# Kernel tuning notes

Hardware: AMD Instinct MI355X
Metric: run time of the kernel (lower is better)

The kernel has to match this reference:

```python
import jax, jax.numpy as jnp
import numpy as np

B, S, D, H = 4, 1024, 1024, 16
E = D // H  # head_dim = 64
N = 2 * H  # number of slots


def _ln(x, g, b, eps=1e-5):
    m = x.mean(-1, keepdims=True)
    v = ((x - m) ** 2).mean(-1, keepdims=True)
    return (x - m) / jnp.sqrt(v + eps) * g + b


def _feat(x):
    # F.elu(x, 1.0) + 1.0
    return jax.nn.elu(x) + 1.0


def setup_inputs() -> dict:
    key = jax.random.key(0)
    ks = jax.random.split(key, 40)
    w = lambda k, shape: jax.random.normal(k, shape, jnp.float32) * 0.02
    z = lambda shape: jnp.zeros(shape, jnp.float32)
    o = lambda shape: jnp.ones(shape, jnp.float32)
    return {
        'x': jax.random.normal(ks[0], (B, S, D), jnp.float32),
        'ln1_g': o(D), 'ln1_b': z(D), 'ln2_g': o(D), 'ln2_b': z(D),
        'Wq': w(ks[1], (D, D)), 'bq': z(D),
        'Wk': w(ks[2], (D, D)), 'bk': z(D),
        'Wv': w(ks[3], (D, D)), 'bv': z(D),
        'Wf': w(ks[4], (D, D)), 'bf': z(D),
        'Wr1': w(ks[5], (D, 2 * D)), 'br1': z(2 * D),
        'Wr2': w(ks[6], (2 * D, D)), 'br2': z(D),
        'Wip': w(ks[7], (D, N * E)), 'bip': z(N * E),
        'Wtq': w(ks[8], (E, E)), 'btq': z(E),
        'Wtk': w(ks[9], (E, E)), 'btk': z(E),
        'Wtv': w(ks[10], (E, E)), 'btv': z(E),
        'lnp_g': o(E), 'lnp_b': z(E),
        'Wl1': w(ks[11], (E, 2 * E)), 'bl1': z(2 * E),
        'Wl2': w(ks[12], (2 * E, E)), 'bl2': z(E),
        'Wsp': w(ks[13], (2 * E, E)), 'bsp': z(E),
    }


def reference(x, ln1_g, ln1_b, ln2_g, ln2_b, Wq, bq, Wk, bk, Wv, bv, Wf, bf,
              Wr1, br1, Wr2, br2, Wip, bip, Wtq, btq, Wtk, btk, Wtv, btv,
              lnp_g, lnp_b, Wl1, bl1, Wl2, bl2, Wsp, bsp):
    xn = _ln(x, ln1_g, ln1_b)
    # main q/k/v
    q = (xn @ Wq + bq).reshape(B, S, H, E).transpose(0, 2, 1, 3) / np.sqrt(E)  # [B,H,S,E]
    k = (xn @ Wk + bk).reshape(B, S, H, E)
    v = (xn @ Wv + bv).reshape(B, S, H, E)
    kv0 = jnp.concatenate([k, v], axis=2)  # [B,S,2H,E] initial slots

    # --- competitive (slot) attention, 3 iterations ---
    inp = (xn @ Wip + bip).reshape(B, S, N, E)
    kk = _feat(inp @ Wtk + btk)          # [B,S,N,E]
    vv = inp @ Wtv + btv                 # [B,S,N,E]
    slots = kv0
    scale = 1.0 / E                      # slot_size = head_dim
    for _ in range(3):
        qq = (slots @ Wtq + btq) + kv0
        qq = _feat(qq * (E ** -0.5))
        logits = jnp.einsum('bswe,bsne->bswn', kk, qq)
        attn = jax.nn.softmax(logits, axis=3) + 1e-6
        attn = attn / attn.sum(axis=2, keepdims=True)
        upd = jnp.einsum('bswn,bswe->bsne', attn, vv)
        h = _ln(upd, lnp_g, lnp_b)
        h = jax.nn.relu(h @ Wl1 + bl1) @ Wl2 + bl2
        slots = slots + h * scale
    # slot_dropout is eval-mode identity
    slots = jnp.concatenate([kv0, slots], axis=-1) @ Wsp + bsp  # [B,S,2H,E]

    k2 = slots[:, :, :H].transpose(0, 2, 3, 1)  # [B,H,E,S]
    v2 = slots[:, :, H:].transpose(0, 2, 1, 3)  # [B,H,S,E]
    qf = _feat(q)
    kf = _feat(k2)
    score = qf @ kf                              # [B,H,S,S]
    score = score / (score.sum(-1, keepdims=True) + 1e-5)
    out = (score @ v2).transpose(0, 2, 1, 3).reshape(B, S, D)
    out = out @ Wf + bf
    out = x + out
    res = out
    h = _ln(out, ln2_g, ln2_b)
    h = jax.nn.relu(h @ Wr1 + br1) @ Wr2 + br2  # dropouts are eval-mode identity
    return res + h
```

## Files before the change

### kernel.cpp

```cpp
#include <hip/hip_runtime.h>
#include <hip/hip_bf16.h>

typedef __hip_bfloat16 bf16t;
typedef short short8 __attribute__((ext_vector_type(8)));
typedef float f32x4 __attribute__((ext_vector_type(4)));


__device__ __forceinline__ float featf(float x) { return x > 0.f ? x + 1.f : expf(x); }
__device__ __forceinline__ float ldf(const bf16t* p, size_t i) { return __bfloat162float(p[i]); }
__device__ __forceinline__ float ldf(const float* p, size_t i) { return p[i]; }
__device__ __forceinline__ void stf(bf16t* p, size_t i, float v) { p[i] = __float2bfloat16(v); }
__device__ __forceinline__ void stf(float* p, size_t i, float v) { p[i] = v; }
__device__ __forceinline__ float b2f(unsigned short u) {
    unsigned int x = ((unsigned int)u) << 16; float f; __builtin_memcpy(&f, &x, 4); return f;
}
__device__ __forceinline__ unsigned short f2b(float f) {
    bf16t h = __float2bfloat16(f); unsigned short u; __builtin_memcpy(&u, &h, 2); return u;
}
__device__ __forceinline__ void gl_lds16(const short* g, short* l) {
    __builtin_amdgcn_global_load_lds((const __attribute__((address_space(1))) unsigned int*)g,
                                     (__attribute__((address_space(3))) unsigned int*)l, 16, 0, 0);
}
#define MFMA16(a, b, c) __builtin_amdgcn_mfma_f32_16x16x32_bf16((a), (b), (c), 0, 0, 0)

__global__ __launch_bounds__(256) void fill_k(float* __restrict__ out, int n, float v) {
    int i = blockIdx.x * 256 + threadIdx.x;
    if (i < n) out[i] = v;
}

__global__ __launch_bounds__(256) void transpose_k(const float* __restrict__ W,
                                                   bf16t* __restrict__ Wt,
                                                   int R, int C) {
    __shared__ bf16t tile[32][33];
    int c0 = blockIdx.x * 32, r0 = blockIdx.y * 32;
    int tx = threadIdx.x, ty = threadIdx.y;
    #pragma unroll
    for (int i = 0; i < 32; i += 8) {
        int r = r0 + ty + i, c = c0 + tx;
        if (r < R && c < C) tile[ty + i][tx] = __float2bfloat16(W[(size_t)r * C + c]);
    }
    __syncthreads();
    #pragma unroll
    for (int i = 0; i < 32; i += 8) {
        int r = c0 + ty + i, c = r0 + tx;
        if (r < C && c < R) Wt[(size_t)r * R + c] = tile[tx][ty + i];
    }
}

__global__ __launch_bounds__(256) void small_prep_k(const float* __restrict__ Wtk,
                                                    const float* __restrict__ Wtv,
                                                    const float* __restrict__ Wtq,
                                                    const float* __restrict__ Wl1,
                                                    const float* __restrict__ Wl2,
                                                    const float* __restrict__ Wsp,
                                                    const float* __restrict__ bk,
                                                    const float* __restrict__ bv,
                                                    const float* __restrict__ bip,
                                                    const float* __restrict__ bq,
                                                    bf16t* __restrict__ WtkT,
                                                    bf16t* __restrict__ WtvT,
                                                    bf16t* __restrict__ WtqI,
                                                    bf16t* __restrict__ Wl1T,
                                                    bf16t* __restrict__ Wl2T,
                                                    bf16t* __restrict__ WspT,
                                                    float* __restrict__ bcat) {
    int b = blockIdx.x, tid = threadIdx.x;
    if (b == 0) {
        for (int i = tid; i < 4096; i += 256) { int c = i >> 6, r = i & 63; WtkT[i] = __float2bfloat16(Wtk[r * 64 + c]); }
    } else if (b == 1) {
        for (int i = tid; i < 4096; i += 256) { int c = i >> 6, r = i & 63; WtvT[i] = __float2bfloat16(Wtv[r * 64 + c]); }
    } else if (b == 2) {
        for (int i = tid; i < 8192; i += 256) {
            int e = i >> 7, k = i & 127;
            float v = (k < 64) ? Wtq[k * 64 + e] : ((k - 64 == e) ? 1.f : 0.f);
            WtqI[i] = __float2bfloat16(v);
        }
    } else if (b == 3) {
        for (int i = tid; i < 8192; i += 256) { int n = i >> 6, k = i & 63; Wl1T[i] = __float2bfloat16(Wl1[k * 128 + n]); }
    } else if (b == 4) {
        for (int i = tid; i < 8192; i += 256) { int n = i >> 7, k = i & 127; Wl2T[i] = __float2bfloat16(Wl2[k * 64 + n]); }
    } else if (b == 5) {
        for (int i = tid; i < 8192; i += 256) { int n = i >> 7, k = i & 127; WspT[i] = __float2bfloat16(Wsp[k * 64 + n]); }
    } else {
        for (int i = tid; i < 5120; i += 256) {
            float v;
            if (i < 1024) v = bk[i];
            else if (i < 2048) v = bv[i - 1024];
            else if (i < 4096) v = bip[i - 2048];
            else v = bq[i - 4096];
            bcat[i] = v;
        }
    }
}

__global__ __launch_bounds__(256) void ln_kernel(const float* __restrict__ X,
                                                 const float* __restrict__ g,
                                                 const float* __restrict__ b,
                                                 bf16t* __restrict__ Y) {
    int t = blockIdx.x, tid = threadIdx.x;
    size_t base = (size_t)t * 1024 + tid * 4;
    float v0 = X[base + 0], v1 = X[base + 1], v2 = X[base + 2], v3 = X[base + 3];
    float s = v0 + v1 + v2 + v3;
    float q = v0 * v0 + v1 * v1 + v2 * v2 + v3 * v3;
    __shared__ float rs[4], rq[4];
    for (int o = 32; o > 0; o >>= 1) { s += __shfl_down(s, o); q += __shfl_down(q, o); }
    int wid = tid >> 6, lane = tid & 63;
    if (lane == 0) { rs[wid] = s; rq[wid] = q; }
    __syncthreads();
    float S = rs[0] + rs[1] + rs[2] + rs[3];
    float Q = rq[0] + rq[1] + rq[2] + rq[3];
    float mean = S * (1.f / 1024.f);
    float var = Q * (1.f / 1024.f) - mean * mean;
    float rstd = rsqrtf(var + 1e-5f);
    int c = tid * 4;
    stf(Y, base + 0, (v0 - mean) * rstd * g[c + 0] + b[c + 0]);
    stf(Y, base + 1, (v1 - mean) * rstd * g[c + 1] + b[c + 1]);
    stf(Y, base + 2, (v2 - mean) * rstd * g[c + 2] + b[c + 2]);
    stf(Y, base + 3, (v3 - mean) * rstd * g[c + 3] + b[c + 3]);
}

template <int MODE, typename TC, typename TADD>
__global__ __launch_bounds__(256) void gemm128_k(const bf16t* __restrict__ A,
                                                 const bf16t* __restrict__ Bt,
                                                 const float* __restrict__ bias,
                                                 const TADD* __restrict__ add,
                                                 TC* __restrict__ C,
                                                 int M, int N, int K, int ldC) {
    __shared__ short As[128 * 32];
    __shared__ short Bs[128 * 32];
    int tid = threadIdx.x;
    int wave = tid >> 6, lane = tid & 63;
    int l16 = lane & 15, quad = lane >> 4;
    int tilesM = M >> 7;
    int tm = blockIdx.x % tilesM;
    int tn = blockIdx.x / tilesM;
    int wm = wave >> 1, wn = wave & 1;

    int lrow = lane >> 2;
    int lseg = (lane & 3) * 8;
    const short* Ag = (const short*)A + (size_t)(tm * 128 + wave * 32 + lrow) * K + lseg;
    const short* Ag2 = Ag + (size_t)16 * K;
    const short* Bg = (const short*)Bt + (size_t)(tn * 128 + wave * 32 + lrow) * K + lseg;
    const short* Bg2 = Bg + (size_t)16 * K;
    short* Asw = As + (wave * 32) * 32;
    short* Asw2 = Asw + 16 * 32;
    short* Bsw = Bs + (wave * 32) * 32;
    short* Bsw2 = Bsw + 16 * 32;

    f32x4 acc[4][4] = {};
    for (int k0 = 0; k0 < K; k0 += 32) {
        gl_lds16(Ag + k0, Asw);
        gl_lds16(Ag2 + k0, Asw2);
        gl_lds16(Bg + k0, Bsw);
        gl_lds16(Bg2 + k0, Bsw2);
        __syncthreads();
        short8 av[4], bv[4];
        #pragma unroll
        for (int i = 0; i < 4; i++)
            av[i] = *(const short8*)(As + (wm * 64 + i * 16 + l16) * 32 + quad * 8);
        #pragma unroll
        for (int j = 0; j < 4; j++)
            bv[j] = *(const short8*)(Bs + (wn * 64 + j * 16 + l16) * 32 + quad * 8);
        #pragma unroll
        for (int i = 0; i < 4; i++)
            #pragma unroll
            for (int j = 0; j < 4; j++)
                acc[i][j] = MFMA16(av[i], bv[j], acc[i][j]);
        __syncthreads();
    }

    #pragma unroll
    for (int j = 0; j < 4; j++) {
        int col = tn * 128 + wn * 64 + j * 16 + l16;
        float bcol = bias[col];
        #pragma unroll
        for (int i = 0; i < 4; i++) {
            int row0 = tm * 128 + wm * 64 + i * 16 + quad * 4;
            #pragma unroll
            for (int r = 0; r < 4; r++) {
                int row = row0 + r;
                float v = acc[i][j][r] + bcol;
                float outv;
                if constexpr (MODE == 0) outv = v;
                else if constexpr (MODE == 4) outv = fmaxf(v, 0.f);
                else if constexpr (MODE == 5) outv = v + ldf(add, (size_t)row * N + col);
                else outv = v;
                stf(C, (size_t)row * ldC + col, outv);
            }
        }
    }
}

__global__ __launch_bounds__(256) void gemm_proj_k(const bf16t* __restrict__ A,
                                                   const bf16t* __restrict__ Bt,
                                                   const float* __restrict__ bias,
                                                   bf16t* __restrict__ kv0,
                                                   bf16t* __restrict__ inp,
                                                   bf16t* __restrict__ qf) {
    __shared__ short As[128 * 32];
    __shared__ short Bs[128 * 32];
    const int K = 1024;
    int tid = threadIdx.x;
    int wave = tid >> 6, lane = tid & 63;
    int l16 = lane & 15, quad = lane >> 4;
    int tm = blockIdx.x & 31;
    int tn = blockIdx.x >> 5;
    int wm = wave >> 1, wn = wave & 1;

    int lrow = lane >> 2;
    int lseg = (lane & 3) * 8;
    const short* Ag = (const short*)A + (size_t)(tm * 128 + wave * 32 + lrow) * K + lseg;
    const short* Ag2 = Ag + (size_t)16 * K;
    const short* Bg = (const short*)Bt + (size_t)(tn * 128 + wave * 32 + lrow) * K + lseg;
    const short* Bg2 = Bg + (size_t)16 * K;
    short* Asw = As + (wave * 32) * 32;
    short* Asw2 = Asw + 16 * 32;
    short* Bsw = Bs + (wave * 32) * 32;
    short* Bsw2 = Bsw + 16 * 32;

    f32x4 acc[4][4] = {};
    for (int k0 = 0; k0 < K; k0 += 32) {
        gl_lds16(Ag + k0, Asw);
        gl_lds16(Ag2 + k0, Asw2);
        gl_lds16(Bg + k0, Bsw);
        gl_lds16(Bg2 + k0, Bsw2);
        __syncthreads();
        short8 av[4], bv[4];
        #pragma unroll
        for (int i = 0; i < 4; i++)
            av[i] = *(const short8*)(As + (wm * 64 + i * 16 + l16) * 32 + quad * 8);
        #pragma unroll
        for (int j = 0; j < 4; j++)
            bv[j] = *(const short8*)(Bs + (wn * 64 + j * 16 + l16) * 32 + quad * 8);
        #pragma unroll
        for (int i = 0; i < 4; i++)
            #pragma unroll
            for (int j = 0; j < 4; j++)
                acc[i][j] = MFMA16(av[i], bv[j], acc[i][j]);
        __syncthreads();
    }

    #pragma unroll
    for (int j = 0; j < 4; j++) {
        int col = tn * 128 + wn * 64 + j * 16 + l16;
        float bcol = bias[col];
        #pragma unroll
        for (int i = 0; i < 4; i++) {
            int row0 = tm * 128 + wm * 64 + i * 16 + quad * 4;
            #pragma unroll
            for (int r = 0; r < 4; r++) {
                int row = row0 + r;
                float v = acc[i][j][r] + bcol;
                if (tn < 16) stf(kv0, (size_t)row * 2048 + col, v);
                else if (tn < 32) stf(inp, (size_t)row * 2048 + (col - 2048), v);
                else stf(qf, (size_t)row * 1024 + (col - 4096), featf(v * 0.125f));
            }
        }
    }
}

template <int MODE, typename TC>
__global__ __launch_bounds__(256) void gemm_k(const bf16t* __restrict__ A,
                                              const bf16t* __restrict__ Bt,
                                              const float* __restrict__ bias,
                                              TC* __restrict__ C,
                                              int M, int N, int K, int ldC) {
    int wave = threadIdx.x >> 6;
    int lane = threadIdx.x & 63;
    int tilesN = N >> 6;
    int tiles = (M >> 6) * tilesN;
    int tile = blockIdx.x * 4 + wave;
    if (tile >= tiles) return;
    int tm = tile / tilesN, tn = tile - tm * tilesN;
    int l16 = lane & 15, quad = lane >> 4;

    f32x4 acc[4][4] = {};
    const short* Ab = (const short*)A + (size_t)(tm * 64 + l16) * K;
    const short* Bb = (const short*)Bt + (size_t)(tn * 64 + l16) * K;

    for (int k0 = 0; k0 < K; k0 += 32) {
        int ka = k0 + quad * 8;
        short8 av[4], bv[4];
        #pragma unroll
        for (int i = 0; i < 4; i++) av[i] = *(const short8*)(Ab + (size_t)i * 16 * K + ka);
        #pragma unroll
        for (int j = 0; j < 4; j++) bv[j] = *(const short8*)(Bb + (size_t)j * 16 * K + ka);
        #pragma unroll
        for (int i = 0; i < 4; i++)
            #pragma unroll
            for (int j = 0; j < 4; j++)
                acc[i][j] = MFMA16(av[i], bv[j], acc[i][j]);
    }

    #pragma unroll
    for (int j = 0; j < 4; j++) {
        int col = tn * 64 + j * 16 + l16;
        float bcol = bias[col];
        #pragma unroll
        for (int i = 0; i < 4; i++) {
            int row0 = tm * 64 + i * 16 + quad * 4;
            #pragma unroll
            for (int r = 0; r < 4; r++) {
                int row = row0 + r;
                float v = acc[i][j][r] + bcol;
                if constexpr (MODE == 7) {
                    stf(C, (size_t)(row >> 5) * 2048 + (size_t)col * 32 + (row & 31), v);
                } else {
                    float outv;
                    if constexpr (MODE == 0) outv = v;
                    else if constexpr (MODE == 1) outv = featf(v);
                    else outv = v;
                    stf(C, (size_t)row * ldC + col, outv);
                }
            }
        }
    }
}

__global__ __launch_bounds__(256) void gemm_cat_k(const bf16t* __restrict__ A1,
                                                  const bf16t* __restrict__ A2,
                                                  const bf16t* __restrict__ Bt,
                                                  const float* __restrict__ bias,
                                                  bf16t* __restrict__ C, int M) {
    int wave = threadIdx.x >> 6;
    int lane = threadIdx.x & 63;
    int tiles = M >> 6;
    int tile = blockIdx.x * 4 + wave;
    if (tile >= tiles) return;
    int tm = tile;
    int l16 = lane & 15, quad = lane >> 4;
    f32x4 acc[4][4] = {};
    #pragma unroll
    for (int p = 0; p < 2; p++) {
        const short* Ab = (const short*)(p ? A2 : A1) + (size_t)(tm * 64 + l16) * 64;
        const short* Bb = (const short*)Bt + (size_t)l16 * 128 + p * 64;
        #pragma unroll
        for (int k0 = 0; k0 < 64; k0 += 32) {
            int ka = k0 + quad * 8;
            short8 av[4], bv[4];
            #pragma unroll
            for (int i = 0; i < 4; i++) av[i] = *(const short8*)(Ab + (size_t)i * 16 * 64 + ka);
            #pragma unroll
            for (int j = 0; j < 4; j++) bv[j] = *(const short8*)(Bb + (size_t)j * 16 * 128 + ka);
            #pragma unroll
            for (int i = 0; i < 4; i++)
                #pragma unroll
                for (int j = 0; j < 4; j++)
                    acc[i][j] = MFMA16(av[i], bv[j], acc[i][j]);
        }
    }
    #pragma unroll
    for (int j = 0; j < 4; j++) {
        int col = j * 16 + l16;
        float bcol = bias[col];
        #pragma unroll
        for (int i = 0; i < 4; i++) {
            int row0 = tm * 64 + i * 16 + quad * 4;
            #pragma unroll
            for (int r = 0; r < 4; r++)
                C[(size_t)(row0 + r) * 64 + col] = __float2bfloat16(acc[i][j][r] + bcol);
        }
    }
}

__global__ __launch_bounds__(256) void slot_all_k(const bf16t* __restrict__ kv0,
                                                  const bf16t* __restrict__ kk,
                                                  const bf16t* __restrict__ vvT,
                                                  const bf16t* __restrict__ WtqI,
                                                  const float* __restrict__ btq,
                                                  const float* __restrict__ lnpg,
                                                  const float* __restrict__ lnpb,
                                                  const bf16t* __restrict__ Wl1T,
                                                  const float* __restrict__ bl1,
                                                  const bf16t* __restrict__ Wl2T,
                                                  const float* __restrict__ bl2,
                                                  bf16t* __restrict__ slots_out) {
    __shared__ short slotsS[4][32 * 72];
    __shared__ short scratch[4][32 * 72];
    int wave = threadIdx.x >> 6, lane = threadIdx.x & 63;
    int l16 = lane & 15, quad = lane >> 4;
    int t = blockIdx.x * 4 + wave;
    short* S = slotsS[wave];
    short* X = scratch[wave];
    size_t tbase = (size_t)t * 2048;

    {
        const short* src = (const short*)kv0 + tbase;
        #pragma unroll
        for (int p = 0; p < 4; p++) {
            int idx = p * 512 + lane * 8;
            int row = idx >> 6, col = idx & 63;
            *(short8*)(S + row * 72 + col) = *(const short8*)(src + idx);
        }
    }
    short8 kkf[2][2], kvf[2][2];
    #pragma unroll
    for (int i = 0; i < 2; i++)
        #pragma unroll
        for (int k0 = 0; k0 < 2; k0++) {
            size_t fo = tbase + (size_t)(i * 16 + l16) * 64 + k0 * 32 + quad * 8;
            kkf[i][k0] = *(const short8*)((const short*)kk + fo);
            kvf[i][k0] = *(const short8*)((const short*)kv0 + fo);
        }

    float btqv[4], bl2v[4], lgv[4], lbv[4], bl1v[8];
    #pragma unroll
    for (int j = 0; j < 4; j++) {
        btqv[j] = btq[j * 16 + l16]; bl2v[j] = bl2[j * 16 + l16];
        lgv[j] = lnpg[j * 16 + l16]; lbv[j] = lnpb[j * 16 + l16];
    }
    #pragma unroll
    for (int j = 0; j < 8; j++) bl1v[j] = bl1[j * 16 + l16];

    for (int it = 0; it < 3; it++) {
        f32x4 aq[2][4] = {};
        #pragma unroll
        for (int k0 = 0; k0 < 4; k0++) {
            short8 af[2];
            #pragma unroll
            for (int i = 0; i < 2; i++)
                af[i] = (k0 < 2) ? *(const short8*)(S + (i * 16 + l16) * 72 + k0 * 32 + quad * 8)
                                 : kvf[i][k0 - 2];
            #pragma unroll
            for (int j = 0; j < 4; j++) {
                short8 bf_ = *(const short8*)((const short*)WtqI + (size_t)(j * 16 + l16) * 128 + k0 * 32 + quad * 8);
                #pragma unroll
                for (int i = 0; i < 2; i++) aq[i][j] = MFMA16(af[i], bf_, aq[i][j]);
            }
        }
        #pragma unroll
        for (int i = 0; i < 2; i++)
            #pragma unroll
            for (int j = 0; j < 4; j++)
                #pragma unroll
                for (int r = 0; r < 4; r++) {
                    int n = i * 16 + quad * 4 + r, e = j * 16 + l16;
                    X[n * 72 + e] = (short)f2b(featf((aq[i][j][r] + btqv[j]) * 0.125f));
                }
        f32x4 al[2][2] = {};
        #pragma unroll
        for (int k0 = 0; k0 < 2; k0++) {
            short8 bf_[2];
            #pragma unroll
            for (int j = 0; j < 2; j++)
                bf_[j] = *(const short8*)(X + (j * 16 + l16) * 72 + k0 * 32 + quad * 8);
            #pragma unroll
            for (int i = 0; i < 2; i++)
                #pragma unroll
                for (int j = 0; j < 2; j++)
                    al[i][j] = MFMA16(kkf[i][k0], bf_[j], al[i][j]);
        }
        #pragma unroll
        for (int i = 0; i < 2; i++)
            #pragma unroll
            for (int r = 0; r < 4; r++) {
                float m = fmaxf(al[i][0][r], al[i][1][r]);
                #pragma unroll
                for (int d = 1; d < 16; d <<= 1) m = fmaxf(m, __shfl_xor(m, d));
                float e0 = expf(al[i][0][r] - m), e1 = expf(al[i][1][r] - m);
                float s = e0 + e1;
                #pragma unroll
                for (int d = 1; d < 16; d <<= 1) s += __shfl_xor(s, d);
                float inv = 1.f / s;
                al[i][0][r] = e0 * inv + 1e-6f;
                al[i][1][r] = e1 * inv + 1e-6f;
            }
        #pragma unroll
        for (int j = 0; j < 2; j++) {
            float cs = 0.f;
            #pragma unroll
            for (int i = 0; i < 2; i++)
                #pragma unroll
                for (int r = 0; r < 4; r++) cs += al[i][j][r];
            cs += __shfl_xor(cs, 16);
            cs += __shfl_xor(cs, 32);
            float inv = 1.f / cs;
            #pragma unroll
            for (int i = 0; i < 2; i++)
                #pragma unroll
                for (int r = 0; r < 4; r++) al[i][j][r] *= inv;
        }
        #pragma unroll
        for (int i = 0; i < 2; i++)
            #pragma unroll
            for (int j = 0; j < 2; j++)
                #pragma unroll
                for (int r = 0; r < 4; r++) {
                    int w = i * 16 + quad * 4 + r, n = j * 16 + l16;
                    X[n * 40 + w] = (short)f2b(al[i][j][r]);
                }
        f32x4 au[2][4] = {};
        {
            short8 af[2];
            #pragma unroll
            for (int i = 0; i < 2; i++)
                af[i] = *(const short8*)(X + (i * 16 + l16) * 40 + quad * 8);
            #pragma unroll
            for (int j = 0; j < 4; j++) {
                short8 bf_ = *(const short8*)((const short*)vvT + tbase + (size_t)(j * 16 + l16) * 32 + quad * 8);
                #pragma unroll
                for (int i = 0; i < 2; i++) au[i][j] = MFMA16(af[i], bf_, au[i][j]);
            }
        }
        #pragma unroll
        for (int i = 0; i < 2; i++)
            #pragma unroll
            for (int r = 0; r < 4; r++) {
                float s1 = 0.f, s2 = 0.f;
                #pragma unroll
                for (int j = 0; j < 4; j++) { float u = au[i][j][r]; s1 += u; s2 += u * u; }
                #pragma unroll
                for (int d = 1; d < 16; d <<= 1) { s1 += __shfl_xor(s1, d); s2 += __shfl_xor(s2, d); }
                float mean = s1 * (1.f / 64.f);
                float var = s2 * (1.f / 64.f) - mean * mean;
                float rstd = rsqrtf(var + 1e-5f);
                int n = i * 16 + quad * 4 + r;
                #pragma unroll
                for (int j = 0; j < 4; j++)
                    X[n * 72 + j * 16 + l16] = (short)f2b((au[i][j][r] - mean) * rstd * lgv[j] + lbv[j]);
            }
        short8 a1[2][2];
        #pragma unroll
        for (int i = 0; i < 2; i++)
            #pragma unroll
            for (int k0 = 0; k0 < 2; k0++)
                a1[i][k0] = *(const short8*)(X + (i * 16 + l16) * 72 + k0 * 32 + quad * 8);
        f32x4 ac2[2][4] = {};
        #pragma unroll
        for (int c = 0; c < 2; c++) {
            f32x4 ac1[2][4] = {};
            #pragma unroll
            for (int k0 = 0; k0 < 2; k0++)
                #pragma unroll
                for (int j = 0; j < 4; j++) {
                    short8 bf_ = *(const short8*)((const short*)Wl1T + (size_t)((c * 4 + j) * 16 + l16) * 64 + k0 * 32 + quad * 8);
                    #pragma unroll
                    for (int i = 0; i < 2; i++) ac1[i][j] = MFMA16(a1[i][k0], bf_, ac1[i][j]);
                }
            #pragma unroll
            for (int i = 0; i < 2; i++)
                #pragma unroll
                for (int j = 0; j < 4; j++)
                    #pragma unroll
                    for (int r = 0; r < 4; r++) {
                        int n = i * 16 + quad * 4 + r;
                        X[n * 72 + j * 16 + l16] = (short)f2b(fmaxf(ac1[i][j][r] + bl1v[c * 4 + j], 0.f));
                    }
            #pragma unroll
            for (int kc = 0; kc < 2; kc++) {
                short8 a2[2];
                #pragma unroll
                for (int i = 0; i < 2; i++)
                    a2[i] = *(const short8*)(X + (i * 16 + l16) * 72 + kc * 32 + quad * 8);
                int k1 = c * 2 + kc;
                #pragma unroll
                for (int j = 0; j < 4; j++) {
                    short8 bf_ = *(const short8*)((const short*)Wl2T + (size_t)(j * 16 + l16) * 128 + k1 * 32 + quad * 8);
                    #pragma unroll
                    for (int i = 0; i < 2; i++) ac2[i][j] = MFMA16(a2[i], bf_, ac2[i][j]);
                }
            }
        }
        #pragma unroll
        for (int i = 0; i < 2; i++)
            #pragma unroll
            for (int j = 0; j < 4; j++)
                #pragma unroll
                for (int r = 0; r < 4; r++) {
                    int n = i * 16 + quad * 4 + r, e = j * 16 + l16;
                    float old = b2f((unsigned short)S[n * 72 + e]);
                    S[n * 72 + e] = (short)f2b(old + (ac2[i][j][r] + bl2v[j]) * (1.f / 64.f));
                }
    }
    {
        short* dst = (short*)slots_out + tbase;
        #pragma unroll
        for (int p = 0; p < 4; p++) {
            int idx = p * 512 + lane * 8;
            int row = idx >> 6, col = idx & 63;
            *(short8*)(dst + idx) = *(const short8*)(S + row * 72 + col);
        }
    }
}

__global__ __launch_bounds__(256) void kv_outer_k(const bf16t* __restrict__ slotsO,
                                                  float* __restrict__ Kmat,
                                                  float* __restrict__ ksum) {
    __shared__ short kfT[64 * 72];
    __shared__ short v2T[64 * 72];
    __shared__ float ksred[8][64];
    int bh = blockIdx.x;
    int b = bh >> 4, h = bh & 15;
    int tid = threadIdx.x;
    int wave = tid >> 6, lane = tid & 63;
    int l16 = lane & 15, quad = lane >> 4;
    int m0 = wave * 16;

    int sgrp = tid >> 5;
    int e0 = (tid & 31) * 2;
    float ks0 = 0.f, ks1 = 0.f;
    f32x4 acc[4];
    #pragma unroll
    for (int j = 0; j < 4; j++) acc[j] = (f32x4){0.f, 0.f, 0.f, 0.f};

    for (int tile = 0; tile < 16; tile++) {
        #pragma unroll
        for (int p = 0; p < 8; p++) {
            int sl = p * 8 + sgrp;
            size_t row = ((size_t)(b * 1024 + tile * 64 + sl)) * 2048;
            unsigned int dk = *(const unsigned int*)((const unsigned short*)slotsO + row + h * 64 + e0);
            float f0 = featf(b2f((unsigned short)(dk & 0xffff)));
            float f1 = featf(b2f((unsigned short)(dk >> 16)));
            ks0 += f0; ks1 += f1;
            kfT[e0 * 72 + sl] = (short)f2b(f0);
            kfT[(e0 + 1) * 72 + sl] = (short)f2b(f1);
            unsigned int dv = *(const unsigned int*)((const unsigned short*)slotsO + row + (16 + h) * 64 + e0);
            v2T[e0 * 72 + sl] = (short)(dv & 0xffff);
            v2T[(e0 + 1) * 72 + sl] = (short)(dv >> 16);
        }
        __syncthreads();
        #pragma unroll
        for (int k2 = 0; k2 < 2; k2++) {
            short8 a = *(const short8*)(kfT + (m0 + l16) * 72 + k2 * 32 + quad * 8);
            #pragma unroll
            for (int j = 0; j < 4; j++) {
                short8 bv = *(const short8*)(v2T + (j * 16 + l16) * 72 + k2 * 32 + quad * 8);
                acc[j] = MFMA16(a, bv, acc[j]);
            }
        }
        __syncthreads();
    }

    float* Km = Kmat + (size_t)bh * 4096;
    #pragma unroll
    for (int j = 0; j < 4; j++)
        #pragma unroll
        for (int r = 0; r < 4; r++)
            Km[(m0 + quad * 4 + r) * 64 + j * 16 + l16] = acc[j][r];

    ksred[sgrp][e0] = ks0;
    ksred[sgrp][e0 + 1] = ks1;
    __syncthreads();
    if (tid < 64) {
        float s = 0.f;
        #pragma unroll
        for (int r = 0; r < 8; r++) s += ksred[r][tid];
        ksum[bh * 64 + tid] = s;
    }
}

__global__ __launch_bounds__(256) void attn_out_k(const bf16t* __restrict__ qf,
                                                  const float* __restrict__ Kmat,
                                                  const float* __restrict__ ksum,
                                                  bf16t* __restrict__ out) {
    int t = blockIdx.x, tid = threadIdx.x;
    int b = t >> 10;
    __shared__ float q[16 * 65];
    __shared__ float dinv[16];
    for (int i = tid; i < 1024; i += 256) {
        int h = i >> 6, e = i & 63;
        q[h * 65 + e] = __bfloat162float(qf[(size_t)t * 1024 + i]);
    }
    __syncthreads();
    if (tid < 16) {
        int bh = b * 16 + tid;
        float d = 0.f;
        for (int e = 0; e < 64; e++) d += q[tid * 65 + e] * ksum[bh * 64 + e];
        dinv[tid] = 1.f / (d + 1e-5f);
    }
    __syncthreads();
    int h = tid >> 4, j0 = (tid & 15) * 4;
    const float* Km = Kmat + (size_t)(b * 16 + h) * 4096;
    float a0 = 0.f, a1 = 0.f, a2 = 0.f, a3 = 0.f;
    for (int e = 0; e < 64; e++) {
        float qe = q[h * 65 + e];
        const float* kr = Km + e * 64 + j0;
        a0 += qe * kr[0]; a1 += qe * kr[1]; a2 += qe * kr[2]; a3 += qe * kr[3];
    }
    float di = dinv[h];
    size_t ob = (size_t)t * 1024 + h * 64 + j0;
    out[ob + 0] = __float2bfloat16(a0 * di);
    out[ob + 1] = __float2bfloat16(a1 * di);
    out[ob + 2] = __float2bfloat16(a2 * di);
    out[ob + 3] = __float2bfloat16(a3 * di);
}

#define LAUNCH_GEMM(MODE, TCT, A_, Bt_, bias_, C_, M_, N_, K_, ldC_)                         \
    do {                                                                                     \
        int tiles__ = ((M_) >> 6) * ((N_) >> 6);                                             \
        gemm_k<MODE, TCT><<<(tiles__ + 3) / 4, 256, 0, stream>>>(                            \
            (const bf16t*)(A_), (const bf16t*)(Bt_), (const float*)(bias_),                  \
            (TCT*)(C_), (M_), (N_), (K_), (ldC_));                                           \
    } while (0)

#define LAUNCH_GEMM128(MODE, TCT, TADDT, A_, Bt_, bias_, add_, C_, M_, N_, K_, ldC_)         \
    do {                                                                                     \
        int tiles__ = ((M_) >> 7) * ((N_) >> 7);                                             \
        gemm128_k<MODE, TCT, TADDT><<<tiles__, 256, 0, stream>>>(                            \
            (const bf16t*)(A_), (const bf16t*)(Bt_), (const float*)(bias_),                  \
            (const TADDT*)(add_), (TCT*)(C_), (M_), (N_), (K_), (ldC_));                     \
    } while (0)

extern "C" void kernel_launch(void* const* d_in, const int* in_sizes, int n_in,
                              void* d_out, int out_size, void* d_ws, size_t ws_size,
                              hipStream_t stream) {
    (void)in_sizes; (void)n_in;
    const float* x    = (const float*)d_in[0];
    const float* ln1g = (const float*)d_in[1];
    const float* ln1b = (const float*)d_in[2];
    const float* ln2g = (const float*)d_in[3];
    const float* ln2b = (const float*)d_in[4];
    const float* Wq  = (const float*)d_in[5];  const float* bq  = (const float*)d_in[6];
    const float* Wk  = (const float*)d_in[7];  const float* bk  = (const float*)d_in[8];
    const float* Wv  = (const float*)d_in[9];  const float* bv  = (const float*)d_in[10];
    const float* Wf  = (const float*)d_in[11]; const float* bWf = (const float*)d_in[12];
    const float* Wr1 = (const float*)d_in[13]; const float* br1 = (const float*)d_in[14];
    const float* Wr2 = (const float*)d_in[15]; const float* br2 = (const float*)d_in[16];
    const float* Wip = (const float*)d_in[17]; const float* bip = (const float*)d_in[18];
    const float* Wtq = (const float*)d_in[19]; const float* btq = (const float*)d_in[20];
    const float* Wtk = (const float*)d_in[21]; const float* btk = (const float*)d_in[22];
    const float* Wtv = (const float*)d_in[23]; const float* btv = (const float*)d_in[24];
    const float* lnpg= (const float*)d_in[25]; const float* lnpb= (const float*)d_in[26];
    const float* Wl1 = (const float*)d_in[27]; const float* bl1 = (const float*)d_in[28];
    const float* Wl2 = (const float*)d_in[29]; const float* bl2 = (const float*)d_in[30];
    const float* Wsp = (const float*)d_in[31]; const float* bsp = (const float*)d_in[32];

    char* ws = (char*)d_ws;
    size_t off = 0;
    auto alloc = [&](size_t bytes) -> char* {
        off = (off + 255) & ~(size_t)255;
        char* p = ws + off;
        off += bytes;
        return p;
    };
    const size_t T = 4096, TS = 131072;
    const size_t MB8 = T * 1024 * 2, MB16 = T * 2048 * 2;
    bf16t* R_xn   = (bf16t*)alloc(MB8);
    bf16t* R_h1   = (bf16t*)alloc(MB8);
    bf16t* R_kv0  = (bf16t*)alloc(MB16);
    bf16t* R_inp  = (bf16t*)alloc(MB16);
    bf16t* R_kk   = (bf16t*)alloc(MB16);
    bf16t* R_vv   = (bf16t*)alloc(MB16);
    bf16t* R_sl   = (bf16t*)alloc(MB16);
    bf16t* Wcat   = (bf16t*)alloc(5120 * 1024 * 2);
    bf16t* WtkT = (bf16t*)alloc(64 * 64 * 2);
    bf16t* WtvT = (bf16t*)alloc(64 * 64 * 2);
    bf16t* WtqI = (bf16t*)alloc(64 * 128 * 2);
    bf16t* Wl1T = (bf16t*)alloc(128 * 64 * 2);
    bf16t* Wl2T = (bf16t*)alloc(64 * 128 * 2);
    bf16t* WspT = (bf16t*)alloc(64 * 128 * 2);
    float* bcat = (float*)alloc(5120 * 4);
    float* Kmat = (float*)alloc(64 * 4096 * 4);
    float* ksum = (float*)alloc(64 * 64 * 4);

    if (off > ws_size) {
        fill_k<<<(out_size + 255) / 256, 256, 0, stream>>>((float*)d_out, out_size, 1000.f);
        return;
    }
    float* R_res = (float*)R_vv;

    auto tr = [&](const float* W, bf16t* Wt, int R, int C) {
        dim3 g((C + 31) / 32, (R + 31) / 32), blk(32, 8);
        transpose_k<<<g, blk, 0, stream>>>(W, Wt, R, C);
    };

    small_prep_k<<<7, 256, 0, stream>>>(Wtk, Wtv, Wtq, Wl1, Wl2, Wsp, bk, bv, bip, bq,
                                        WtkT, WtvT, WtqI, Wl1T, Wl2T, WspT, bcat);

    ln_kernel<<<4096, 256, 0, stream>>>(x, ln1g, ln1b, R_xn);

    tr(Wk, Wcat, 1024, 1024);
    tr(Wv, Wcat + (size_t)1024 * 1024, 1024, 1024);
    tr(Wip, Wcat + (size_t)2048 * 1024, 1024, 2048);
    tr(Wq, Wcat + (size_t)4096 * 1024, 1024, 1024);

    gemm_proj_k<<<1280, 256, 0, stream>>>(R_xn, Wcat, bcat, R_kv0, R_inp, R_h1);

    LAUNCH_GEMM(1, bf16t, R_inp, WtkT, btk, R_kk, 131072, 64, 64, 64);
    LAUNCH_GEMM(7, bf16t, R_inp, WtvT, btv, R_vv, 131072, 64, 64, 64);

    slot_all_k<<<1024, 256, 0, stream>>>(R_kv0, R_kk, R_vv, WtqI, btq, lnpg, lnpb,
                                         Wl1T, bl1, Wl2T, bl2, R_sl);

    gemm_cat_k<<<512, 256, 0, stream>>>(R_kv0, R_sl, WspT, bsp, R_kk, 131072);

    kv_outer_k<<<64, 256, 0, stream>>>(R_kk, Kmat, ksum);

    attn_out_k<<<4096, 256, 0, stream>>>(R_h1, Kmat, ksum, R_inp);

    tr(Wf, Wcat, 1024, 1024);
    LAUNCH_GEMM128(5, float, float, R_inp, Wcat, bWf, x, R_res, 4096, 1024, 1024, 1024);

    ln_kernel<<<4096, 256, 0, stream>>>(R_res, ln2g, ln2b, R_xn);
    tr(Wr1, Wcat, 1024, 2048);
    LAUNCH_GEMM128(4, bf16t, bf16t, R_xn, Wcat, br1, nullptr, R_sl, 4096, 2048, 1024, 2048);
    tr(Wr2, Wcat, 2048, 1024);
    LAUNCH_GEMM128(5, float, float, R_sl, Wcat, br2, R_res, (float*)d_out, 4096, 1024, 2048, 1024);
}
```

Baseline: 617.0 us.

## Batch weight transposes and fuse kk/vv projections into single kernel launches

Merges the per-matrix transpose launches into two multi-matrix transpose kernels and fuses the two small Wtk/Wtv GEMMs into one kernel that reads the input once and writes both outputs. This cuts launch count and halves reads of the inp tensor. The slot kernel stops keeping kk/kv0 fragments and bias vectors in registers across iterations and reloads them per iteration through a runtime offset, likely to lower register pressure. Transposed FFN weights are placed in the dead kv0 buffer, and the transpose kernel drops its bounds checks, so it assumes dimensions are multiples of 32.

Result: faster. 573.2 us (-7.1%).

```diff
diff --git a/kernel.cpp b/kernel.cpp
--- a/kernel.cpp
+++ b/kernel.cpp
@@ -28,23 +28,29 @@
     if (i < n) out[i] = v;
 }
 
-__global__ __launch_bounds__(256) void transpose_k(const float* __restrict__ W,
-                                                   bf16t* __restrict__ Wt,
-                                                   int R, int C) {
+__global__ __launch_bounds__(256) void multi_transpose_k(const float* __restrict__ s0, const float* __restrict__ s1,
+                                                         const float* __restrict__ s2, const float* __restrict__ s3,
+                                                         bf16t* __restrict__ d0, bf16t* __restrict__ d1,
+                                                         bf16t* __restrict__ d2, bf16t* __restrict__ d3,
+                                                         int R0, int C0, int R1, int C1, int R2, int C2, int R3, int C3,
+                                                         int e0, int e1, int e2) {
     __shared__ bf16t tile[32][33];
-    int c0 = blockIdx.x * 32, r0 = blockIdx.y * 32;
-    int tx = threadIdx.x, ty = threadIdx.y;
-    #pragma unroll
-    for (int i = 0; i < 32; i += 8) {
-        int r = r0 + ty + i, c = c0 + tx;
-        if (r < R && c < C) tile[ty + i][tx] = __float2bfloat16(W[(size_t)r * C + c]);
-    }
+    int b = blockIdx.x;
+    const float* W; bf16t* Wt; int C, R, lb;
+    if (b < e0)      { W = s0; Wt = d0; R = R0; C = C0; lb = b; }
+    else if (b < e1) { W = s1; Wt = d1; R = R1; C = C1; lb = b - e0; }
+    else if (b < e2) { W = s2; Wt = d2; R = R2; C = C2; lb = b - e1; }
+    else             { W = s3; Wt = d3; R = R3; C = C3; lb = b - e2; }
+    int tiles_c = C >> 5;
+    int c0 = (lb % tiles_c) * 32, r0 = (lb / tiles_c) * 32;
+    int tx = threadIdx.x & 31, ty = threadIdx.x >> 5;
+    #pragma unroll
+    for (int i = 0; i < 32; i += 8)
+        tile[ty + i][tx] = __float2bfloat16(W[(size_t)(r0 + ty + i) * C + (c0 + tx)]);
     __syncthreads();
     #pragma unroll
-    for (int i = 0; i < 32; i += 8) {
-        int r = c0 + ty + i, c = r0 + tx;
-        if (r < C && c < R) Wt[(size_t)r * R + c] = tile[tx][ty + i];
-    }
+    for (int i = 0; i < 32; i += 8)
+        Wt[(size_t)(c0 + ty + i) * R + (r0 + tx)] = tile[tx][ty + i];
 }
 
 __global__ __launch_bounds__(256) void small_prep_k(const float* __restrict__ Wtk,
@@ -57,31 +63,35 @@
                                                     const float* __restrict__ bv,
                                                     const float* __restrict__ bip,
                                                     const float* __restrict__ bq,
-                                                    bf16t* __restrict__ WtkT,
-                                                    bf16t* __restrict__ WtvT,
+                                                    const float* __restrict__ btk,
+                                                    const float* __restrict__ btv,
+                                                    bf16t* __restrict__ WtkvT,
                                                     bf16t* __restrict__ WtqI,
                                                     bf16t* __restrict__ Wl1T,
                                                     bf16t* __restrict__ Wl2T,
                                                     bf16t* __restrict__ WspT,
-                                                    float* __restrict__ bcat) {
+                                                    float* __restrict__ bcat,
+                                                    float* __restrict__ bcat2) {
     int b = blockIdx.x, tid = threadIdx.x;
     if (b == 0) {
-        for (int i = tid; i < 4096; i += 256) { int c = i >> 6, r = i & 63; WtkT[i] = __float2bfloat16(Wtk[r * 64 + c]); }
+        for (int i = tid; i < 8192; i += 256) {
+            int n2 = i >> 6, e = i & 63;
+            float v = (n2 < 64) ? Wtk[e * 64 + n2] : Wtv[e * 64 + (n2 - 64)];
+            WtkvT[i] = __float2bfloat16(v);
+        }
     } else if (b == 1) {
-        for (int i = tid; i < 4096; i += 256) { int c = i >> 6, r = i & 63; WtvT[i] = __float2bfloat16(Wtv[r * 64 + c]); }
-    } else if (b == 2) {
         for (int i = tid; i < 8192; i += 256) {
             int e = i >> 7, k = i & 127;
             float v = (k < 64) ? Wtq[k * 64 + e] : ((k - 64 == e) ? 1.f : 0.f);
             WtqI[i] = __float2bfloat16(v);
         }
+    } else if (b == 2) {
+        for (int i = tid; i < 8192; i += 256) { int n = i >> 6, k = i & 63; Wl1T[i] = __float2bfloat16(Wl1[k * 128 + n]); }
     } else if (b == 3) {
-        for (int i = tid; i < 8192; i += 256) { int n = i >> 6, k = i & 63; Wl1T[i] = __float2bfloat16(Wl1[k * 128 + n]); }
+        for (int i = tid; i < 8192; i += 256) { int n = i >> 7, k = i & 127; Wl2T[i] = __float2bfloat16(Wl2[k * 64 + n]); }
     } else if (b == 4) {
-        for (int i = tid; i < 8192; i += 256) { int n = i >> 7, k = i & 127; Wl2T[i] = __float2bfloat16(Wl2[k * 64 + n]); }
+        for (int i = tid; i < 8192; i += 256) { int n = i >> 7, k = i & 127; WspT[i] = __float2bfloat16(Wsp[k * 64 + n]); }
     } else if (b == 5) {
-        for (int i = tid; i < 8192; i += 256) { int n = i >> 7, k = i & 127; WspT[i] = __float2bfloat16(Wsp[k * 64 + n]); }
-    } else {
         for (int i = tid; i < 5120; i += 256) {
             float v;
             if (i < 1024) v = bk[i];
@@ -90,6 +100,8 @@
             else v = bq[i - 4096];
             bcat[i] = v;
         }
+    } else {
+        if (tid < 128) bcat2[tid] = (tid < 64) ? btk[tid] : btv[tid - 64];
     }
 }
 
@@ -259,43 +271,36 @@
     }
 }
 
-template <int MODE, typename TC>
-__global__ __launch_bounds__(256) void gemm_k(const bf16t* __restrict__ A,
-                                              const bf16t* __restrict__ Bt,
-                                              const float* __restrict__ bias,
-                                              TC* __restrict__ C,
-                                              int M, int N, int K, int ldC) {
-    int wave = threadIdx.x >> 6;
-    int lane = threadIdx.x & 63;
-    int tilesN = N >> 6;
-    int tiles = (M >> 6) * tilesN;
+__global__ __launch_bounds__(256) void gemm_kv_k(const bf16t* __restrict__ A,
+                                                 const bf16t* __restrict__ Bt,
+                                                 const float* __restrict__ bias,
+                                                 bf16t* __restrict__ kkO,
+                                                 bf16t* __restrict__ vvTO) {
+    int wave = threadIdx.x >> 6, lane = threadIdx.x & 63;
     int tile = blockIdx.x * 4 + wave;
-    if (tile >= tiles) return;
-    int tm = tile / tilesN, tn = tile - tm * tilesN;
+    int tm = tile >> 1, tn = tile & 1;
     int l16 = lane & 15, quad = lane >> 4;
-
     f32x4 acc[4][4] = {};
-    const short* Ab = (const short*)A + (size_t)(tm * 64 + l16) * K;
-    const short* Bb = (const short*)Bt + (size_t)(tn * 64 + l16) * K;
-
-    for (int k0 = 0; k0 < K; k0 += 32) {
+    const short* Ab = (const short*)A + (size_t)(tm * 64 + l16) * 64;
+    const short* Bb = (const short*)Bt + (size_t)(tn * 64 + l16) * 64;
+    #pragma unroll
+    for (int k0 = 0; k0 < 64; k0 += 32) {
         int ka = k0 + quad * 8;
         short8 av[4], bv[4];
         #pragma unroll
-        for (int i = 0; i < 4; i++) av[i] = *(const short8*)(Ab + (size_t)i * 16 * K + ka);
-        #pragma unroll
-        for (int j = 0; j < 4; j++) bv[j] = *(const short8*)(Bb + (size_t)j * 16 * K + ka);
+        for (int i = 0; i < 4; i++) av[i] = *(const short8*)(Ab + (size_t)i * 16 * 64 + ka);
+        #pragma unroll
+        for (int j = 0; j < 4; j++) bv[j] = *(const short8*)(Bb + (size_t)j * 16 * 64 + ka);
         #pragma unroll
         for (int i = 0; i < 4; i++)
             #pragma unroll
             for (int j = 0; j < 4; j++)
                 acc[i][j] = MFMA16(av[i], bv[j], acc[i][j]);
     }
-
     #pragma unroll
     for (int j = 0; j < 4; j++) {
-        int col = tn * 64 + j * 16 + l16;
-        float bcol = bias[col];
+        int col = j * 16 + l16;
+        float bcol = bias[tn * 64 + col];
         #pragma unroll
         for (int i = 0; i < 4; i++) {
             int row0 = tm * 64 + i * 16 + quad * 4;
@@ -303,15 +308,8 @@
             for (int r = 0; r < 4; r++) {
                 int row = row0 + r;
                 float v = acc[i][j][r] + bcol;
-                if constexpr (MODE == 7) {
-                    stf(C, (size_t)(row >> 5) * 2048 + (size_t)col * 32 + (row & 31), v);
-                } else {
-                    float outv;
-                    if constexpr (MODE == 0) outv = v;
-                    else if constexpr (MODE == 1) outv = featf(v);
-                    else outv = v;
-                    stf(C, (size_t)row * ldC + col, outv);
-                }
+                if (tn == 0) kkO[(size_t)row * 64 + col] = __float2bfloat16(featf(v));
+                else stf(vvTO, (size_t)(row >> 5) * 2048 + (size_t)col * 32 + (row & 31), v);
             }
         }
     }
@@ -374,7 +372,8 @@
                                                   const float* __restrict__ bl1,
                                                   const bf16t* __restrict__ Wl2T,
                                                   const float* __restrict__ bl2,
-                                                  bf16t* __restrict__ slots_out) {
+                                                  bf16t* __restrict__ slots_out,
+                                                  int zoff) {
     __shared__ short slotsS[4][32 * 72];
     __shared__ short scratch[4][32 * 72];
     int wave = threadIdx.x >> 6, lane = threadIdx.x & 63;
@@ -393,54 +392,49 @@
             *(short8*)(S + row * 72 + col) = *(const short8*)(src + idx);
         }
     }
-    short8 kkf[2][2], kvf[2][2];
-    #pragma unroll
-    for (int i = 0; i < 2; i++)
-        #pragma unroll
-        for (int k0 = 0; k0 < 2; k0++) {
-            size_t fo = tbase + (size_t)(i * 16 + l16) * 64 + k0 * 32 + quad * 8;
-            kkf[i][k0] = *(const short8*)((const short*)kk + fo);
-            kvf[i][k0] = *(const short8*)((const short*)kv0 + fo);
-        }
-
-    float btqv[4], bl2v[4], lgv[4], lbv[4], bl1v[8];
-    #pragma unroll
-    for (int j = 0; j < 4; j++) {
-        btqv[j] = btq[j * 16 + l16]; bl2v[j] = bl2[j * 16 + l16];
-        lgv[j] = lnpg[j * 16 + l16]; lbv[j] = lnpb[j * 16 + l16];
-    }
-    #pragma unroll
-    for (int j = 0; j < 8; j++) bl1v[j] = bl1[j * 16 + l16];
-
+
+    #pragma unroll 1
     for (int it = 0; it < 3; it++) {
+        int vo = it * zoff;
         f32x4 aq[2][4] = {};
         #pragma unroll
         for (int k0 = 0; k0 < 4; k0++) {
             short8 af[2];
             #pragma unroll
+            for (int i = 0; i < 2; i++) {
+                if (k0 < 2)
+                    af[i] = *(const short8*)(S + (i * 16 + l16) * 72 + k0 * 32 + quad * 8);
+                else
+                    af[i] = *(const short8*)((const short*)kv0 + tbase + (size_t)((i * 16 + l16) * 64 + (k0 - 2) * 32 + quad * 8 + vo));
+            }
+            #pragma unroll
+            for (int j = 0; j < 4; j++) {
+                short8 bf_ = *(const short8*)((const short*)WtqI + (size_t)((j * 16 + l16) * 128 + k0 * 32 + quad * 8 + vo));
+                #pragma unroll
+                for (int i = 0; i < 2; i++) aq[i][j] = MFMA16(af[i], bf_, aq[i][j]);
+            }
+        }
+        {
+            float btqv[4];
+            #pragma unroll
+            for (int j = 0; j < 4; j++) btqv[j] = btq[j * 16 + l16 + vo];
+            #pragma unroll
             for (int i = 0; i < 2; i++)
-                af[i] = (k0 < 2) ? *(const short8*)(S + (i * 16 + l16) * 72 + k0 * 32 + quad * 8)
-                                 : kvf[i][k0 - 2];
-            #pragma unroll
-            for (int j = 0; j < 4; j++) {
-                short8 bf_ = *(const short8*)((const short*)WtqI + (size_t)(j * 16 + l16) * 128 + k0 * 32 + quad * 8);
-                #pragma unroll
-                for (int i = 0; i < 2; i++) aq[i][j] = MFMA16(af[i], bf_, aq[i][j]);
-            }
-        }
-        #pragma unroll
-        for (int i = 0; i < 2; i++)
-            #pragma unroll
-            for (int j = 0; j < 4; j++)
-                #pragma unroll
-                for (int r = 0; r < 4; r++) {
-                    int n = i * 16 + quad * 4 + r, e = j * 16 + l16;
-                    X[n * 72 + e] = (short)f2b(featf((aq[i][j][r] + btqv[j]) * 0.125f));
-                }
+                #pragma unroll
+                for (int j = 0; j < 4; j++)
+                    #pragma unroll
+                    for (int r = 0; r < 4; r++) {
+                        int n = i * 16 + quad * 4 + r, e = j * 16 + l16;
+                        X[n * 72 + e] = (short)f2b(featf((aq[i][j][r] + btqv[j]) * 0.125f));
+                    }
+        }
         f32x4 al[2][2] = {};
         #pragma unroll
         for (int k0 = 0; k0 < 2; k0++) {
-            short8 bf_[2];
+            short8 ak[2], bf_[2];
+            #pragma unroll
+            for (int i = 0; i < 2; i++)
+                ak[i] = *(const short8*)((const short*)kk + tbase + (size_t)((i * 16 + l16) * 64 + k0 * 32 + quad * 8 + vo));
             #pragma unroll
             for (int j = 0; j < 2; j++)
                 bf_[j] = *(const short8*)(X + (j * 16 + l16) * 72 + k0 * 32 + quad * 8);
@@ -448,7 +442,7 @@
             for (int i = 0; i < 2; i++)
                 #pragma unroll
                 for (int j = 0; j < 2; j++)
-                    al[i][j] = MFMA16(kkf[i][k0], bf_[j], al[i][j]);
+                    al[i][j] = MFMA16(ak[i], bf_[j], al[i][j]);
         }
         #pragma unroll
         for (int i = 0; i < 2; i++)
@@ -497,28 +491,33 @@
                 af[i] = *(const short8*)(X + (i * 16 + l16) * 40 + quad * 8);
             #pragma unroll
             for (int j = 0; j < 4; j++) {
-                short8 bf_ = *(const short8*)((const short*)vvT + tbase + (size_t)(j * 16 + l16) * 32 + quad * 8);
+                short8 bf_ = *(const short8*)((const short*)vvT + tbase + (size_t)((j * 16 + l16) * 32 + quad * 8 + vo));
                 #pragma unroll
                 for (int i = 0; i < 2; i++) au[i][j] = MFMA16(af[i], bf_, au[i][j]);
             }
         }
-        #pragma unroll
-        for (int i = 0; i < 2; i++)
-            #pragma unroll
-            for (int r = 0; r < 4; r++) {
-                float s1 = 0.f, s2 = 0.f;
-                #pragma unroll
-                for (int j = 0; j < 4; j++) { float u = au[i][j][r]; s1 += u; s2 += u * u; }
-                #pragma unroll
-                for (int d = 1; d < 16; d <<= 1) { s1 += __shfl_xor(s1, d); s2 += __shfl_xor(s2, d); }
-                float mean = s1 * (1.f / 64.f);
-                float var = s2 * (1.f / 64.f) - mean * mean;
-                float rstd = rsqrtf(var + 1e-5f);
-                int n = i * 16 + quad * 4 + r;
-                #pragma unroll
-                for (int j = 0; j < 4; j++)
-                    X[n * 72 + j * 16 + l16] = (short)f2b((au[i][j][r] - mean) * rstd * lgv[j] + lbv[j]);
-            }
+        {
+            float lgv[4], lbv[4];
+            #pragma unroll
+            for (int j = 0; j < 4; j++) { lgv[j] = lnpg[j * 16 + l16 + vo]; lbv[j] = lnpb[j * 16 + l16 + vo]; }
+            #pragma unroll
+            for (int i = 0; i < 2; i++)
+                #pragma unroll
+                for (int r = 0; r < 4; r++) {
+                    float s1 = 0.f, s2 = 0.f;
+                    #pragma unroll
+                    for (int j = 0; j < 4; j++) { float u = au[i][j][r]; s1 += u; s2 += u * u; }
+                    #pragma unroll
+                    for (int d = 1; d < 16; d <<= 1) { s1 += __shfl_xor(s1, d); s2 += __shfl_xor(s2, d); }
+                    float mean = s1 * (1.f / 64.f);
+                    float var = s2 * (1.f / 64.f) - mean * mean;
+                    float rstd = rsqrtf(var + 1e-5f);
+                    int n = i * 16 + quad * 4 + r;
+                    #pragma unroll
+                    for (int j = 0; j < 4; j++)
+                        X[n * 72 + j * 16 + l16] = (short)f2b((au[i][j][r] - mean) * rstd * lgv[j] + lbv[j]);
+                }
+        }
         short8 a1[2][2];
         #pragma unroll
         for (int i = 0; i < 2; i++)
@@ -533,44 +532,54 @@
             for (int k0 = 0; k0 < 2; k0++)
                 #pragma unroll
                 for (int j = 0; j < 4; j++) {
-                    short8 bf_ = *(const short8*)((const short*)Wl1T + (size_t)((c * 4 + j) * 16 + l16) * 64 + k0 * 32 + quad * 8);
+                    short8 bf_ = *(const short8*)((const short*)Wl1T + (size_t)(((c * 4 + j) * 16 + l16) * 64 + k0 * 32 + quad * 8 + vo));
                     #pragma unroll
                     for (int i = 0; i < 2; i++) ac1[i][j] = MFMA16(a1[i][k0], bf_, ac1[i][j]);
                 }
+            {
+                float bl1v[4];
+                #pragma unroll
+                for (int j = 0; j < 4; j++) bl1v[j] = bl1[(c * 4 + j) * 16 + l16 + vo];
+                #pragma unroll
+                for (int i = 0; i < 2; i++)
+                    #pragma unroll
+                    for (int j = 0; j < 4; j++)
+                        #pragma unroll
+                        for (int r = 0; r < 4; r++) {
+                            int n = i * 16 + quad * 4 + r;
+                            X[n * 72 + j * 16 + l16] = (short)f2b(fmaxf(ac1[i][j][r] + bl1v[j], 0.f));
+                        }
+            }
+            #pragma unroll
+            for (int kc = 0; kc < 2; kc++) {
+                short8 a2[2];
+                #pragma unroll
+                for (int i = 0; i < 2; i++)
+                    a2[i] = *(const short8*)(X + (i * 16 + l16) * 72 + kc * 32 + quad * 8);
+                int k1 = c * 2 + kc;
+                #pragma unroll
+                for (int j = 0; j < 4; j++) {
+                    short8 bf_ = *(const short8*)((const short*)Wl2T + (size_t)((j * 16 + l16) * 128 + k1 * 32 + quad * 8 + vo));
+                    #pragma unroll
+                    for (int i = 0; i < 2; i++) ac2[i][j] = MFMA16(a2[i], bf_, ac2[i][j]);
+                }
+            }
+        }
+        {
+            float bl2v[4];
+            #pragma unroll
+            for (int j = 0; j < 4; j++) bl2v[j] = bl2[j * 16 + l16 + vo];
             #pragma unroll
             for (int i = 0; i < 2; i++)
                 #pragma unroll
                 for (int j = 0; j < 4; j++)
                     #pragma unroll
                     for (int r = 0; r < 4; r++) {
-                        int n = i * 16 + quad * 4 + r;
-                        X[n * 72 + j * 16 + l16] = (short)f2b(fmaxf(ac1[i][j][r] + bl1v[c * 4 + j], 0.f));
+                        int n = i * 16 + quad * 4 + r, e = j * 16 + l16;
+                        float old = b2f((unsigned short)S[n * 72 + e]);
+                        S[n * 72 + e] = (short)f2b(old + (ac2[i][j][r] + bl2v[j]) * (1.f / 64.f));
                     }
-            #pragma unroll
-            for (int kc = 0; kc < 2; kc++) {
-                short8 a2[2];
-                #pragma unroll
-                for (int i = 0; i < 2; i++)
-                    a2[i] = *(const short8*)(X + (i * 16 + l16) * 72 + kc * 32 + quad * 8);
-                int k1 = c * 2 + kc;
-                #pragma unroll
-                for (int j = 0; j < 4; j++) {
-                    short8 bf_ = *(const short8*)((const short*)Wl2T + (size_t)(j * 16 + l16) * 128 + k1 * 32 + quad * 8);
-                    #pragma unroll
-                    for (int i = 0; i < 2; i++) ac2[i][j] = MFMA16(a2[i], bf_, ac2[i][j]);
-                }
-            }
-        }
-        #pragma unroll
-        for (int i = 0; i < 2; i++)
-            #pragma unroll
-            for (int j = 0; j < 4; j++)
-                #pragma unroll
-                for (int r = 0; r < 4; r++) {
-                    int n = i * 16 + quad * 4 + r, e = j * 16 + l16;
-                    float old = b2f((unsigned short)S[n * 72 + e]);
-                    S[n * 72 + e] = (short)f2b(old + (ac2[i][j][r] + bl2v[j]) * (1.f / 64.f));
-                }
+        }
     }
     {
         short* dst = (short*)slots_out + tbase;
@@ -684,14 +693,6 @@
     out[ob + 2] = __float2bfloat16(a2 * di);
     out[ob + 3] = __float2bfloat16(a3 * di);
 }
-
-#define LAUNCH_GEMM(MODE, TCT, A_, Bt_, bias_, C_, M_, N_, K_, ldC_)                         \
-    do {                                                                                     \
-        int tiles__ = ((M_) >> 6) * ((N_) >> 6);                                             \
-        gemm_k<MODE, TCT><<<(tiles__ + 3) / 4, 256, 0, stream>>>(                            \
-            (const bf16t*)(A_), (const bf16t*)(Bt_), (const float*)(bias_),                  \
-            (TCT*)(C_), (M_), (N_), (K_), (ldC_));                                           \
-    } while (0)
 
 #define LAUNCH_GEMM128(MODE, TCT, TADDT, A_, Bt_, bias_, add_, C_, M_, N_, K_, ldC_)         \
     do {                                                                                     \
@@ -743,13 +744,13 @@
     bf16t* R_vv   = (bf16t*)alloc(MB16);
     bf16t* R_sl   = (bf16t*)alloc(MB16);
     bf16t* Wcat   = (bf16t*)alloc(5120 * 1024 * 2);
-    bf16t* WtkT = (bf16t*)alloc(64 * 64 * 2);
-    bf16t* WtvT = (bf16t*)alloc(64 * 64 * 2);
+    bf16t* WtkvT = (bf16t*)alloc(128 * 64 * 2);
     bf16t* WtqI = (bf16t*)alloc(64 * 128 * 2);
     bf16t* Wl1T = (bf16t*)alloc(128 * 64 * 2);
     bf16t* Wl2T = (bf16t*)alloc(64 * 128 * 2);
     bf16t* WspT = (bf16t*)alloc(64 * 128 * 2);
     float* bcat = (float*)alloc(5120 * 4);
+    float* bcat2 = (float*)alloc(128 * 4);
     float* Kmat = (float*)alloc(64 * 4096 * 4);
     float* ksum = (float*)alloc(64 * 64 * 4);
 
@@ -758,42 +759,43 @@
         return;
     }
     float* R_res = (float*)R_vv;
-
-    auto tr = [&](const float* W, bf16t* Wt, int R, int C) {
-        dim3 g((C + 31) / 32, (R + 31) / 32), blk(32, 8);
-        transpose_k<<<g, blk, 0, stream>>>(W, Wt, R, C);
-    };
-
-    small_prep_k<<<7, 256, 0, stream>>>(Wtk, Wtv, Wtq, Wl1, Wl2, Wsp, bk, bv, bip, bq,
-                                        WtkT, WtvT, WtqI, Wl1T, Wl2T, WspT, bcat);
+    bf16t* WfT  = R_kv0;
+    bf16t* Wr1T = R_kv0 + (size_t)1024 * 1024;
+    bf16t* Wr2T = R_kv0 + (size_t)3072 * 1024;
+
+    small_prep_k<<<7, 256, 0, stream>>>(Wtk, Wtv, Wtq, Wl1, Wl2, Wsp, bk, bv, bip, bq, btk, btv,
+                                        WtkvT, WtqI, Wl1T, Wl2T, WspT, bcat, bcat2);
 
     ln_kernel<<<4096, 256, 0, stream>>>(x, ln1g, ln1b, R_xn);
 
-    tr(Wk, Wcat, 1024, 1024);
-    tr(Wv, Wcat + (size_t)1024 * 1024, 1024, 1024);
-    tr(Wip, Wcat + (size_t)2048 * 1024, 1024, 2048);
-    tr(Wq, Wcat + (size_t)4096 * 1024, 1024, 1024);
+    multi_transpose_k<<<5120, 256, 0, stream>>>(
+        Wk, Wv, Wip, Wq,
+        Wcat, Wcat + (size_t)1024 * 1024, Wcat + (size_t)2048 * 1024, Wcat + (size_t)4096 * 1024,
+        1024, 1024, 1024, 1024, 1024, 2048, 1024, 1024,
+        1024, 2048, 4096);
 
     gemm_proj_k<<<1280, 256, 0, stream>>>(R_xn, Wcat, bcat, R_kv0, R_inp, R_h1);
 
-    LAUNCH_GEMM(1, bf16t, R_inp, WtkT, btk, R_kk, 131072, 64, 64, 64);
-    LAUNCH_GEMM(7, bf16t, R_inp, WtvT, btv, R_vv, 131072, 64, 64, 64);
+    gemm_kv_k<<<1024, 256, 0, stream>>>(R_inp, WtkvT, bcat2, R_kk, R_vv);
 
     slot_all_k<<<1024, 256, 0, stream>>>(R_kv0, R_kk, R_vv, WtqI, btq, lnpg, lnpb,
-                                         Wl1T, bl1, Wl2T, bl2, R_sl);
+                                         Wl1T, bl1, Wl2T, bl2, R_sl, 0);
 
     gemm_cat_k<<<512, 256, 0, stream>>>(R_kv0, R_sl, WspT, bsp, R_kk, 131072);
 
+    multi_transpose_k<<<5120, 256, 0, stream>>>(
+        Wf, Wr1, Wr2, Wr2,
+        WfT, Wr1T, Wr2T, Wr2T,
+        1024, 1024, 1024, 2048, 2048, 1024, 2048, 1024,
+        1024, 3072, 5120);
+
     kv_outer_k<<<64, 256, 0, stream>>>(R_kk, Kmat, ksum);
 
     attn_out_k<<<4096, 256, 0, stream>>>(R_h1, Kmat, ksum, R_inp);
 
-    tr(Wf, Wcat, 1024, 1024);
-    LAUNCH_GEMM128(5, float, float, R_inp, Wcat, bWf, x, R_res, 4096, 1024, 1024, 1024);
+    LAUNCH_GEMM128(5, float, float, R_inp, WfT, bWf, x, R_res, 4096, 1024, 1024, 1024);
 
     ln_kernel<<<4096, 256, 0, stream>>>(R_res, ln2g, ln2b, R_xn);
-    tr(Wr1, Wcat, 1024, 2048);
-    LAUNCH_GEMM128(4, bf16t, bf16t, R_xn, Wcat, br1, nullptr, R_sl, 4096, 2048, 1024, 2048);
-    tr(Wr2, Wcat, 2048, 1024);
-    LAUNCH_GEMM128(5, float, float, R_sl, Wcat, br2, R_res, (float*)d_out, 4096, 1024, 2048, 1024);
-}
+    LAUNCH_GEMM128(4, bf16t, bf16t, R_xn, Wr1T, br1, nullptr, R_sl, 4096, 2048, 1024, 2048);
+    LAUNCH_GEMM128(5, float, float, R_sl, Wr2T, br2, R_res, (float*)d_out, 4096, 1024, 2048, 1024);
+}
```
